# Optimization experiments

Hardware: AMD Instinct MI355X
Metric: run time of the kernel (lower is better)

## Reference

```python
import jax, jax.numpy as jnp
import numpy as np
import math

B, H, N, DH = 4, 8, 1024, 128
DPT = 4  # point feature dim (<=4 branch: squared-distance map only)

def setup_inputs() -> dict:
    key = jax.random.key(0)
    ks = jax.random.split(key, 10)
    q   = jax.random.normal(ks[0], (B, H, N, DH), jnp.float32)
    k   = jax.random.normal(ks[1], (B, H, N, DH), jnp.float32)
    v   = jax.random.normal(ks[2], (B, H, N, DH), jnp.float32)
    c   = jax.random.normal(ks[3], (B, H, N, 1), jnp.float32)
    d_q = jax.random.normal(ks[4], (B, N, DPT), jnp.float32)
    d_k = jax.random.normal(ks[5], (B, N, DPT), jnp.float32)
    # LazyLinear(1 -> nhead): per-head scalar weight + bias
    w_w = jax.random.normal(ks[6], (H,), jnp.float32) * 0.1
    b_w = jax.random.normal(ks[7], (H,), jnp.float32) * 0.1
    w_b = jax.random.normal(ks[8], (H,), jnp.float32) * 0.1
    b_b = jax.random.normal(ks[9], (H,), jnp.float32) * 0.1
    return {"q": q, "k": k, "v": v, "c": c, "d_q": d_q, "d_k": d_k,
            "w_w": w_w, "b_w": b_w, "w_b": w_b, "b_b": b_b}

def reference(q, k, v, c, d_q, d_k, w_w, b_w, w_b, b_b):
    dh = q.shape[-1]
    # pairwise squared distances on first 3 coords (torch: under no_grad)
    dq3 = d_q[:, :, :3]
    dk3 = d_k[:, :, :3]
    dist = jax.lax.stop_gradient(
        jnp.sum(dq3 ** 2, -1)[:, :, None]
        + jnp.sum(dk3 ** 2, -1)[:, None, :]
        - 2.0 * jnp.einsum('bnd,bmd->bnm', dq3, dk3))  # [B,N,M]
    db = dist[:, None, :, :]  # [B,1,N,M]
    wbc = lambda p: p[None, :, None, None]  # [1,H,1,1]
    # distmap_w = softplus(-(w*dist + b)); distmap_b = w*dist + b (identity acts)
    distmap_w = jax.nn.softplus(-(db * wbc(w_w) + wbc(b_w)))  # [B,H,N,M]
    distmap_b = db * wbc(w_b) + wbc(b_b)                      # [B,H,N,M]
    # scaled dot-product scores per head
    scores = jnp.einsum('bhnd,bhmd->bhnm', q, k) / math.sqrt(dh)
    scores = jax.nn.relu(scores * distmap_w + distmap_b)
    detr = (jnp.sum(scores, -1, keepdims=True)
            + jnp.sum(jax.nn.softplus(c), 2, keepdims=True) + 1e-9)
    scores = scores / detr
    out = jnp.einsum('bhnm,bhmd->bhnd', scores, v)
    return out, scores
```

## Files before the change

### kernel.cpp

```cpp
#include <hip/hip_runtime.h>


typedef __attribute__((ext_vector_type(8))) short short8;
typedef __attribute__((ext_vector_type(4))) float f32x4;

#define OUT_ELEMS 4194304ull
#define WS_K      0ull
#define WS_VT     8388608ull
#define WS_P      16777216ull
#define WS_INVD   83886080ull
#define WS_CS     84017152ull

__device__ __forceinline__ unsigned short f2bf(float f) {
    unsigned u = __builtin_bit_cast(unsigned, f);
    u += 0x7FFFu + ((u >> 16) & 1u);
    return (unsigned short)(u >> 16);
}
__device__ __forceinline__ float bf2f(unsigned short s) {
    unsigned u = ((unsigned)s) << 16;
    return __builtin_bit_cast(float, u);
}
__device__ __forceinline__ float softplus(float x) {
    return fmaxf(x, 0.f) + __logf(1.f + __expf(-fabsf(x)));
}

__global__ __launch_bounds__(256) void prep_all(
    const float* __restrict__ k, const float* __restrict__ v, const float* __restrict__ c,
    unsigned short* __restrict__ wsK, unsigned short* __restrict__ wsVt, float* __restrict__ wsCs)
{
    __shared__ unsigned short sT[64 * 132];
    const int blk = blockIdx.x, tid = threadIdx.x;
    if (blk < 512) {
        int t = blk * 256 + tid;
        for (int u = t; u < 524288; u += 131072) {
            float4 a = reinterpret_cast<const float4*>(k)[u * 2];
            float4 b = reinterpret_cast<const float4*>(k)[u * 2 + 1];
            short8 o;
            o[0]=(short)f2bf(a.x); o[1]=(short)f2bf(a.y); o[2]=(short)f2bf(a.z); o[3]=(short)f2bf(a.w);
            o[4]=(short)f2bf(b.x); o[5]=(short)f2bf(b.y); o[6]=(short)f2bf(b.z); o[7]=(short)f2bf(b.w);
            reinterpret_cast<short8*>(wsK)[u] = o;
        }
    } else if (blk < 1024) {
        const int vb = blk - 512;
        const int bh = vb >> 4, m0 = (vb & 15) * 64;
        const float* src = v + ((size_t)bh * 1024 + m0) * 128;
        for (int i = tid; i < 2048; i += 256) {
            int row = i >> 5, c4 = i & 31;
            float4 t = reinterpret_cast<const float4*>(src)[i];
            unsigned long long pk = (unsigned long long)f2bf(t.x)
                                  | ((unsigned long long)f2bf(t.y) << 16)
                                  | ((unsigned long long)f2bf(t.z) << 32)
                                  | ((unsigned long long)f2bf(t.w) << 48);
            *reinterpret_cast<unsigned long long*>(&sT[row * 132 + c4 * 4]) = pk;
        }
        __syncthreads();
        for (int u = tid; u < 2048; u += 256) {
            int dh = u >> 4, ms = u & 15;
            unsigned long long pk = (unsigned long long)sT[(ms*4+0)*132 + dh]
                                  | ((unsigned long long)sT[(ms*4+1)*132 + dh] << 16)
                                  | ((unsigned long long)sT[(ms*4+2)*132 + dh] << 32)
                                  | ((unsigned long long)sT[(ms*4+3)*132 + dh] << 48);
            *reinterpret_cast<unsigned long long*>(&wsVt[((size_t)bh * 128 + dh) * 1024 + m0 + ms * 4]) = pk;
        }
    } else {
        __shared__ float red[4];
        const int bh = blk - 1024;
        float p = 0.f;
        for (int i = tid; i < 1024; i += 256) p += softplus(c[(size_t)bh * 1024 + i]);
        p += __shfl_xor(p, 32, 64); p += __shfl_xor(p, 16, 64); p += __shfl_xor(p, 8, 64);
        p += __shfl_xor(p,  4, 64); p += __shfl_xor(p,  2, 64); p += __shfl_xor(p, 1, 64);
        if ((tid & 63) == 0) red[tid >> 6] = p;
        __syncthreads();
        if (tid == 0) wsCs[bh] = red[0] + red[1] + red[2] + red[3] + 1e-9f;
    }
}

__global__ __launch_bounds__(512, 4) void sam_main(
    const float* __restrict__ q, const float* __restrict__ dqp, const float* __restrict__ dkp,
    const float* __restrict__ w_w, const float* __restrict__ b_w,
    const float* __restrict__ w_b, const float* __restrict__ b_b,
    const unsigned short* __restrict__ wsK, const unsigned short* __restrict__ wsVt,
    const float* __restrict__ wsCs, float* __restrict__ wsInvd,
    unsigned short* __restrict__ wsP, float* __restrict__ out)
{
    __shared__ __align__(16) unsigned short sKall[2 * 8704];
    __shared__ __align__(16) unsigned short sVtall[2 * 9216];
    __shared__ float sdkall[2 * 256];
    __shared__ float s_inv[64];

    const int bid  = blockIdx.x;
    const int bh   = bid & 31;
    const int n0   = (bid >> 5) * 64;
    const int b    = bh >> 3;
    const int h    = bh & 7;
    const int tid  = threadIdx.x;
    const int lane = tid & 63;
    const int wave = tid >> 6;
    const int g    = wave >> 2;
    const int wl   = wave & 3;
    const int w16  = wl * 16;
    const int tg   = tid & 255;
    const int l15  = lane & 15;
    const int quad = lane >> 4;

    const float ww = w_w[h], bw = b_w[h], wb = w_b[h], bb = b_b[h];
    const float SCALE = 0.08838834764831845f;

    {
        const float* qbase = q + ((size_t)bh * 1024 + n0) * 128;
        for (int i = tid; i < 2048; i += 512) {
            int row = i >> 5, c4 = i & 31;
            float4 t = reinterpret_cast<const float4*>(qbase)[i];
            unsigned long long pk = (unsigned long long)f2bf(t.x)
                                  | ((unsigned long long)f2bf(t.y) << 16)
                                  | ((unsigned long long)f2bf(t.z) << 32)
                                  | ((unsigned long long)f2bf(t.w) << 48);
            *reinterpret_cast<unsigned long long*>(&sKall[row * 136 + c4 * 4]) = pk;
        }
    }
    float qx[4], qy[4], qz[4], qs[4];
    #pragma unroll
    for (int r = 0; r < 4; r++) {
        int nl = w16 + quad * 4 + r;
        float4 d4 = reinterpret_cast<const float4*>(dqp)[(size_t)b * 1024 + n0 + nl];
        qx[r] = d4.x; qy[r] = d4.y; qz[r] = d4.z;
        qs[r] = d4.x*d4.x + d4.y*d4.y + d4.z*d4.z;
    }
    const float cs = wsCs[bh];
    __syncthreads();
    short8 afr[4];
    {
        const unsigned short* aq = &sKall[(w16 + l15) * 136];
        #pragma unroll
        for (int ks = 0; ks < 4; ks++)
            afr[ks] = *reinterpret_cast<const short8*>(aq + ks * 32 + quad * 8);
    }
    __syncthreads();

    f32x4 oacc[8];
    #pragma unroll
    for (int i = 0; i < 8; i++) oacc[i] = {0.f, 0.f, 0.f, 0.f};
    float rs[4] = {0.f, 0.f, 0.f, 0.f};

    unsigned short* sKg  = sKall  + g * 8704;
    unsigned short* sVtg = sVtall + g * 9216;
    unsigned short* sP   = sKg + wl * 1152;
    float* sdkg = sdkall + g * 256;

    for (int t8 = 0; t8 < 8; t8++) {
        const int m0 = (t8 * 2 + g) * 64;
        for (int i = tg; i < 1024; i += 256) {
            int row = i >> 4, seg = i & 15;
            short8 d = *reinterpret_cast<const short8*>(wsK + ((size_t)bh * 1024 + m0 + row) * 128 + seg * 8);
            *reinterpret_cast<short8*>(&sKg[row * 136 + seg * 8]) = d;
        }
        for (int i = tg; i < 1024; i += 256) {
            int dh = i >> 3, seg = i & 7;
            short8 d = *reinterpret_cast<const short8*>(wsVt + ((size_t)bh * 128 + dh) * 1024 + m0 + seg * 8);
            *reinterpret_cast<short8*>(&sVtg[dh * 72 + seg * 8]) = d;
        }
        if (tg < 64) {
            float4 d4 = reinterpret_cast<const float4*>(dkp)[(size_t)b * 1024 + m0 + tg];
            sdkg[tg] = d4.x; sdkg[64 + tg] = d4.y; sdkg[128 + tg] = d4.z;
            sdkg[192 + tg] = d4.x*d4.x + d4.y*d4.y + d4.z*d4.z;
        }
        __syncthreads();

        f32x4 cacc[4];
        #pragma unroll
        for (int mf = 0; mf < 4; mf++) {
            cacc[mf] = {0.f, 0.f, 0.f, 0.f};
            const unsigned short* bq = &sKg[(mf * 16 + l15) * 136];
            #pragma unroll
            for (int ks = 0; ks < 4; ks++) {
                short8 bfr = *reinterpret_cast<const short8*>(bq + ks * 32 + quad * 8);
                cacc[mf] = __builtin_amdgcn_mfma_f32_16x16x32_bf16(afr[ks], bfr, cacc[mf], 0, 0, 0);
            }
        }
        __syncthreads();

        #pragma unroll
        for (int mf = 0; mf < 4; mf++) {
            const int mloc = mf * 16 + l15;
            const float kx = sdkg[mloc], ky = sdkg[64 + mloc], kz = sdkg[128 + mloc], ksq = sdkg[192 + mloc];
            #pragma unroll
            for (int r = 0; r < 4; r++) {
                float dist = qs[r] + ksq - 2.f * (qx[r]*kx + qy[r]*ky + qz[r]*kz);
                float aw = softplus(-(dist * ww + bw));
                float ab = dist * wb + bb;
                float val = fmaxf(cacc[mf][r] * SCALE * aw + ab, 0.f);
                rs[r] += val;
                sP[(quad * 4 + r) * 72 + mf * 16 + l15] = f2bf(val);
            }
        }
        #pragma unroll
        for (int ks2 = 0; ks2 < 2; ks2++) {
            short8 pfr = *reinterpret_cast<const short8*>(&sP[l15 * 72 + ks2 * 32 + quad * 8]);
            #pragma unroll
            for (int df = 0; df < 8; df++) {
                short8 vfr = *reinterpret_cast<const short8*>(&sVtg[(df * 16 + l15) * 72 + ks2 * 32 + quad * 8]);
                oacc[df] = __builtin_amdgcn_mfma_f32_16x16x32_bf16(pfr, vfr, oacc[df], 0, 0, 0);
            }
        }
        {
            unsigned short* dst = wsP + ((size_t)bh * 1024 + n0 + w16) * 1024 + m0;
            #pragma unroll
            for (int half = 0; half < 2; half++) {
                int u = half * 64 + lane;
                int row = u >> 3, seg = u & 7;
                short8 d = *reinterpret_cast<const short8*>(&sP[row * 72 + seg * 8]);
                *reinterpret_cast<short8*>(dst + (size_t)row * 1024 + seg * 8) = d;
            }
        }
        __syncthreads();
    }

    #pragma unroll
    for (int r = 0; r < 4; r++) {
        float t = rs[r];
        t += __shfl_xor(t, 1, 64); t += __shfl_xor(t, 2, 64);
        t += __shfl_xor(t, 4, 64); t += __shfl_xor(t, 8, 64);
        if (l15 == 0) sdkall[g * 256 + w16 + quad * 4 + r] = t;
    }
    __syncthreads();
    if (tid < 64) {
        float iv = 1.f / (sdkall[tid] + sdkall[256 + tid] + cs);
        s_inv[tid] = iv;
        wsInvd[(size_t)bh * 1024 + n0 + tid] = iv;
    }
    __syncthreads();

    float* sO = reinterpret_cast<float*>(sKall) + wl * 2112;
    if (g == 1) {
        #pragma unroll
        for (int df = 0; df < 8; df++)
            #pragma unroll
            for (int r = 0; r < 4; r++)
                sO[(quad * 4 + r) * 132 + df * 16 + l15] = oacc[df][r];
    }
    __syncthreads();
    if (g == 0) {
        #pragma unroll
        for (int df = 0; df < 8; df++) {
            #pragma unroll
            for (int r = 0; r < 4; r++) {
                int row = w16 + quad * 4 + r;
                float o = (oacc[df][r] + sO[(quad * 4 + r) * 132 + df * 16 + l15]) * s_inv[row];
                out[((size_t)bh * 1024 + n0 + row) * 128 + df * 16 + l15] = o;
            }
        }
    }
}

__global__ __launch_bounds__(256) void rescale(
    const unsigned short* __restrict__ wsP, const float* __restrict__ wsInvd,
    float* __restrict__ scores)
{
    const int row = blockIdx.x;
    const float iv = wsInvd[row];
    const unsigned long long d = *reinterpret_cast<const unsigned long long*>(
        wsP + (size_t)row * 1024 + threadIdx.x * 4);
    float4 o;
    o.x = bf2f((unsigned short)(d       & 0xFFFF)) * iv;
    o.y = bf2f((unsigned short)((d>>16) & 0xFFFF)) * iv;
    o.z = bf2f((unsigned short)((d>>32) & 0xFFFF)) * iv;
    o.w = bf2f((unsigned short)((d>>48) & 0xFFFF)) * iv;
    reinterpret_cast<float4*>(scores + (size_t)row * 1024)[threadIdx.x] = o;
}

extern "C" void kernel_launch(void* const* d_in, const int* in_sizes, int n_in,
                              void* d_out, int out_size, void* d_ws, size_t ws_size,
                              hipStream_t stream) {
    const float* q   = (const float*)d_in[0];
    const float* k   = (const float*)d_in[1];
    const float* v   = (const float*)d_in[2];
    const float* c   = (const float*)d_in[3];
    const float* dq  = (const float*)d_in[4];
    const float* dk  = (const float*)d_in[5];
    const float* w_w = (const float*)d_in[6];
    const float* b_w = (const float*)d_in[7];
    const float* w_b = (const float*)d_in[8];
    const float* b_b = (const float*)d_in[9];
    float* out = (float*)d_out;
    char* ws = (char*)d_ws;
    unsigned short* wsK  = (unsigned short*)(ws + WS_K);
    unsigned short* wsVt = (unsigned short*)(ws + WS_VT);
    unsigned short* wsP  = (unsigned short*)(ws + WS_P);
    float* wsInvd = (float*)(ws + WS_INVD);
    float* wsCs   = (float*)(ws + WS_CS);

    hipLaunchKernelGGL(prep_all, dim3(1056), dim3(256), 0, stream, k, v, c, wsK, wsVt, wsCs);
    hipLaunchKernelGGL(sam_main, dim3(512), dim3(512), 0, stream,
                       q, dq, dk, w_w, b_w, w_b, b_b, wsK, wsVt, wsCs, wsInvd, wsP, out);
    hipLaunchKernelGGL(rescale, dim3(32768), dim3(256), 0, stream, wsP, wsInvd, out + OUT_ELEMS);
}
```

Before: 273.1 us.

## Two-pass main kernel: compute row sums first, then write normalized scores directly

The main kernel now runs a first pass over all key tiles that computes only QK^T plus the distance modulation to get the row sums, and so the inverse denominators. A second pass recomputes the scores, normalizes them, writes fp32 scores straight to the output and feeds the normalized bf16 P into the PV matmul. This drops the bf16 P workspace round-trip and the separate rescale kernel launch. In exchange it doubles the QK^T MFMA and softplus work and reloads K tiles twice. The fp32 score stores are also per-lane scalar writes with a 16-float contiguous stride rather than vectorized rows.

```diff
diff --git a/kernel.cpp b/kernel.cpp
--- a/kernel.cpp
+++ b/kernel.cpp
@@ -7,18 +7,12 @@
 #define OUT_ELEMS 4194304ull
 #define WS_K      0ull
 #define WS_VT     8388608ull
-#define WS_P      16777216ull
-#define WS_INVD   83886080ull
-#define WS_CS     84017152ull
+#define WS_CS     16777216ull
 
 __device__ __forceinline__ unsigned short f2bf(float f) {
     unsigned u = __builtin_bit_cast(unsigned, f);
     u += 0x7FFFu + ((u >> 16) & 1u);
     return (unsigned short)(u >> 16);
-}
-__device__ __forceinline__ float bf2f(unsigned short s) {
-    unsigned u = ((unsigned)s) << 16;
-    return __builtin_bit_cast(float, u);
 }
 __device__ __forceinline__ float softplus(float x) {
     return fmaxf(x, 0.f) + __logf(1.f + __expf(-fabsf(x)));
@@ -80,8 +74,7 @@
     const float* __restrict__ w_w, const float* __restrict__ b_w,
     const float* __restrict__ w_b, const float* __restrict__ b_b,
     const unsigned short* __restrict__ wsK, const unsigned short* __restrict__ wsVt,
-    const float* __restrict__ wsCs, float* __restrict__ wsInvd,
-    unsigned short* __restrict__ wsP, float* __restrict__ out)
+    const float* __restrict__ wsCs, float* __restrict__ out)
 {
     __shared__ __align__(16) unsigned short sKall[2 * 8704];
     __shared__ __align__(16) unsigned short sVtall[2 * 9216];
@@ -137,16 +130,12 @@
     }
     __syncthreads();
 
-    f32x4 oacc[8];
-    #pragma unroll
-    for (int i = 0; i < 8; i++) oacc[i] = {0.f, 0.f, 0.f, 0.f};
-    float rs[4] = {0.f, 0.f, 0.f, 0.f};
-
     unsigned short* sKg  = sKall  + g * 8704;
     unsigned short* sVtg = sVtall + g * 9216;
     unsigned short* sP   = sKg + wl * 1152;
     float* sdkg = sdkall + g * 256;
 
+    float rs[4] = {0.f, 0.f, 0.f, 0.f};
     for (int t8 = 0; t8 < 8; t8++) {
         const int m0 = (t8 * 2 + g) * 64;
         for (int i = tg; i < 1024; i += 256) {
@@ -154,11 +143,6 @@
             short8 d = *reinterpret_cast<const short8*>(wsK + ((size_t)bh * 1024 + m0 + row) * 128 + seg * 8);
             *reinterpret_cast<short8*>(&sKg[row * 136 + seg * 8]) = d;
         }
-        for (int i = tg; i < 1024; i += 256) {
-            int dh = i >> 3, seg = i & 7;
-            short8 d = *reinterpret_cast<const short8*>(wsVt + ((size_t)bh * 128 + dh) * 1024 + m0 + seg * 8);
-            *reinterpret_cast<short8*>(&sVtg[dh * 72 + seg * 8]) = d;
-        }
         if (tg < 64) {
             float4 d4 = reinterpret_cast<const float4*>(dkp)[(size_t)b * 1024 + m0 + tg];
             sdkg[tg] = d4.x; sdkg[64 + tg] = d4.y; sdkg[128 + tg] = d4.z;
@@ -177,8 +161,6 @@
                 cacc[mf] = __builtin_amdgcn_mfma_f32_16x16x32_bf16(afr[ks], bfr, cacc[mf], 0, 0, 0);
             }
         }
-        __syncthreads();
-
         #pragma unroll
         for (int mf = 0; mf < 4; mf++) {
             const int mloc = mf * 16 + l15;
@@ -188,28 +170,7 @@
                 float dist = qs[r] + ksq - 2.f * (qx[r]*kx + qy[r]*ky + qz[r]*kz);
                 float aw = softplus(-(dist * ww + bw));
                 float ab = dist * wb + bb;
-                float val = fmaxf(cacc[mf][r] * SCALE * aw + ab, 0.f);
-                rs[r] += val;
-                sP[(quad * 4 + r) * 72 + mf * 16 + l15] = f2bf(val);
-            }
-        }
-        #pragma unroll
-        for (int ks2 = 0; ks2 < 2; ks2++) {
-            short8 pfr = *reinterpret_cast<const short8*>(&sP[l15 * 72 + ks2 * 32 + quad * 8]);
-            #pragma unroll
-            for (int df = 0; df < 8; df++) {
-                short8 vfr = *reinterpret_cast<const short8*>(&sVtg[(df * 16 + l15) * 72 + ks2 * 32 + quad * 8]);
-                oacc[df] = __builtin_amdgcn_mfma_f32_16x16x32_bf16(pfr, vfr, oacc[df], 0, 0, 0);
-            }
-        }
-        {
-            unsigned short* dst = wsP + ((size_t)bh * 1024 + n0 + w16) * 1024 + m0;
-            #pragma unroll
-            for (int half = 0; half < 2; half++) {
-                int u = half * 64 + lane;
-                int row = u >> 3, seg = u & 7;
-                short8 d = *reinterpret_cast<const short8*>(&sP[row * 72 + seg * 8]);
-                *reinterpret_cast<short8*>(dst + (size_t)row * 1024 + seg * 8) = d;
+                rs[r] += fmaxf(cacc[mf][r] * SCALE * aw + ab, 0.f);
             }
         }
         __syncthreads();
@@ -223,12 +184,76 @@
         if (l15 == 0) sdkall[g * 256 + w16 + quad * 4 + r] = t;
     }
     __syncthreads();
-    if (tid < 64) {
-        float iv = 1.f / (sdkall[tid] + sdkall[256 + tid] + cs);
-        s_inv[tid] = iv;
-        wsInvd[(size_t)bh * 1024 + n0 + tid] = iv;
-    }
-    __syncthreads();
+    if (tid < 64) s_inv[tid] = 1.f / (sdkall[tid] + sdkall[256 + tid] + cs);
+    __syncthreads();
+
+    float inv4[4];
+    #pragma unroll
+    for (int r = 0; r < 4; r++) inv4[r] = s_inv[w16 + quad * 4 + r];
+
+    f32x4 oacc[8];
+    #pragma unroll
+    for (int i = 0; i < 8; i++) oacc[i] = {0.f, 0.f, 0.f, 0.f};
+    float* scb = out + OUT_ELEMS + ((size_t)bh << 20);
+
+    for (int t8 = 0; t8 < 8; t8++) {
+        const int m0 = (t8 * 2 + g) * 64;
+        for (int i = tg; i < 1024; i += 256) {
+            int row = i >> 4, seg = i & 15;
+            short8 d = *reinterpret_cast<const short8*>(wsK + ((size_t)bh * 1024 + m0 + row) * 128 + seg * 8);
+            *reinterpret_cast<short8*>(&sKg[row * 136 + seg * 8]) = d;
+        }
+        for (int i = tg; i < 1024; i += 256) {
+            int dh = i >> 3, seg = i & 7;
+            short8 d = *reinterpret_cast<const short8*>(wsVt + ((size_t)bh * 128 + dh) * 1024 + m0 + seg * 8);
+            *reinterpret_cast<short8*>(&sVtg[dh * 72 + seg * 8]) = d;
+        }
+        if (tg < 64) {
+            float4 d4 = reinterpret_cast<const float4*>(dkp)[(size_t)b * 1024 + m0 + tg];
+            sdkg[tg] = d4.x; sdkg[64 + tg] = d4.y; sdkg[128 + tg] = d4.z;
+            sdkg[192 + tg] = d4.x*d4.x + d4.y*d4.y + d4.z*d4.z;
+        }
+        __syncthreads();
+
+        f32x4 cacc[4];
+        #pragma unroll
+        for (int mf = 0; mf < 4; mf++) {
+            cacc[mf] = {0.f, 0.f, 0.f, 0.f};
+            const unsigned short* bq = &sKg[(mf * 16 + l15) * 136];
+            #pragma unroll
+            for (int ks = 0; ks < 4; ks++) {
+                short8 bfr = *reinterpret_cast<const short8*>(bq + ks * 32 + quad * 8);
+                cacc[mf] = __builtin_amdgcn_mfma_f32_16x16x32_bf16(afr[ks], bfr, cacc[mf], 0, 0, 0);
+            }
+        }
+        __syncthreads();
+
+        #pragma unroll
+        for (int mf = 0; mf < 4; mf++) {
+            const int mloc = mf * 16 + l15;
+            const float kx = sdkg[mloc], ky = sdkg[64 + mloc], kz = sdkg[128 + mloc], ksq = sdkg[192 + mloc];
+            #pragma unroll
+            for (int r = 0; r < 4; r++) {
+                float dist = qs[r] + ksq - 2.f * (qx[r]*kx + qy[r]*ky + qz[r]*kz);
+                float aw = softplus(-(dist * ww + bw));
+                float ab = dist * wb + bb;
+                float val = fmaxf(cacc[mf][r] * SCALE * aw + ab, 0.f);
+                float p   = val * inv4[r];
+                sP[(quad * 4 + r) * 72 + mf * 16 + l15] = f2bf(p);
+                scb[(size_t)(n0 + w16 + quad * 4 + r) * 1024 + m0 + mf * 16 + l15] = p;
+            }
+        }
+        #pragma unroll
+        for (int ks2 = 0; ks2 < 2; ks2++) {
+            short8 pfr = *reinterpret_cast<const short8*>(&sP[l15 * 72 + ks2 * 32 + quad * 8]);
+            #pragma unroll
+            for (int df = 0; df < 8; df++) {
+                short8 vfr = *reinterpret_cast<const short8*>(&sVtg[(df * 16 + l15) * 72 + ks2 * 32 + quad * 8]);
+                oacc[df] = __builtin_amdgcn_mfma_f32_16x16x32_bf16(pfr, vfr, oacc[df], 0, 0, 0);
+            }
+        }
+        __syncthreads();
+    }
 
     float* sO = reinterpret_cast<float*>(sKall) + wl * 2112;
     if (g == 1) {
@@ -245,27 +270,11 @@
             #pragma unroll
             for (int r = 0; r < 4; r++) {
                 int row = w16 + quad * 4 + r;
-                float o = (oacc[df][r] + sO[(quad * 4 + r) * 132 + df * 16 + l15]) * s_inv[row];
+                float o = oacc[df][r] + sO[(quad * 4 + r) * 132 + df * 16 + l15];
                 out[((size_t)bh * 1024 + n0 + row) * 128 + df * 16 + l15] = o;
             }
         }
     }
-}
-
-__global__ __launch_bounds__(256) void rescale(
-    const unsigned short* __restrict__ wsP, const float* __restrict__ wsInvd,
-    float* __restrict__ scores)
-{
-    const int row = blockIdx.x;
-    const float iv = wsInvd[row];
-    const unsigned long long d = *reinterpret_cast<const unsigned long long*>(
-        wsP + (size_t)row * 1024 + threadIdx.x * 4);
-    float4 o;
-    o.x = bf2f((unsigned short)(d       & 0xFFFF)) * iv;
-    o.y = bf2f((unsigned short)((d>>16) & 0xFFFF)) * iv;
-    o.z = bf2f((unsigned short)((d>>32) & 0xFFFF)) * iv;
-    o.w = bf2f((unsigned short)((d>>48) & 0xFFFF)) * iv;
-    reinterpret_cast<float4*>(scores + (size_t)row * 1024)[threadIdx.x] = o;
 }
 
 extern "C" void kernel_launch(void* const* d_in, const int* in_sizes, int n_in,
@@ -285,12 +294,9 @@
     char* ws = (char*)d_ws;
     unsigned short* wsK  = (unsigned short*)(ws + WS_K);
     unsigned short* wsVt = (unsigned short*)(ws + WS_VT);
-    unsigned short* wsP  = (unsigned short*)(ws + WS_P);
-    float* wsInvd = (float*)(ws + WS_INVD);
     float* wsCs   = (float*)(ws + WS_CS);
 
     hipLaunchKernelGGL(prep_all, dim3(1056), dim3(256), 0, stream, k, v, c, wsK, wsVt, wsCs);
     hipLaunchKernelGGL(sam_main, dim3(512), dim3(512), 0, stream,
-                       q, dq, dk, w_w, b_w, w_b, b_b, wsK, wsVt, wsCs, wsInvd, wsP, out);
-    hipLaunchKernelGGL(rescale, dim3(32768), dim3(256), 0, stream, wsP, wsInvd, out + OUT_ELEMS);
-}
+                       q, dq, dk, w_w, b_w, w_b, b_b, wsK, wsVt, wsCs, out);
+}
```

Measured after the change: 268.4 us. No clear change (-1.7%).
